# Optimization experiments

Measured on AMD Instinct MI355X. Metric: run time of the kernel, lower is better.

Reference implementation:

```python
import jax, jax.numpy as jnp
import numpy as np
import math

EMBED_DIM = 2048
NUM_HEADS = 16
DEPTH = 12
HEAD_DIM = EMBED_DIM // NUM_HEADS // 2  # 64
LAMBDA_INIT = 0.8 - 0.6 * math.exp(-0.3 * DEPTH)
EPS = 1e-8


def apply_rope(x):
    # x: (b, s, h, d) -- lucidrains interleaved rotary, freqs_for='lang', theta=10000
    b, s, h, d = x.shape
    inv_freq = 1.0 / (10000.0 ** (jnp.arange(0, d, 2, dtype=jnp.float32) / d))
    t = jnp.arange(s, dtype=jnp.float32)
    freqs = t[:, None] * inv_freq[None, :]           # (s, d/2)
    freqs = jnp.repeat(freqs, 2, axis=-1)            # (s, d) pairwise repeat
    cos = jnp.cos(freqs)[None, :, None, :].astype(x.dtype)
    sin = jnp.sin(freqs)[None, :, None, :].astype(x.dtype)
    x1 = x[..., 0::2]
    x2 = x[..., 1::2]
    rot = jnp.stack([-x2, x1], axis=-1).reshape(x.shape)  # rotate_half, interleaved
    return x * cos + rot * sin


def causal_attn(q, k, v):
    # q,k: (b, s, h, d); v: (b, s, h, e). flash_attn_func default scale = d**-0.5
    b, s, h, d = q.shape
    scale = d ** -0.5
    scores = jnp.einsum('bqhd,bkhd->bhqk', q, k) * scale
    mask = jnp.tril(jnp.ones((s, s), dtype=bool))
    scores = jnp.where(mask[None, None], scores, jnp.finfo(scores.dtype).min)
    p = jax.nn.softmax(scores, axis=-1)
    return jnp.einsum('bhqk,bkhe->bqhe', p, v)


def rms_norm(x, w, b):
    var = jnp.mean(jnp.square(x), axis=-1, keepdims=True)
    return x * jax.lax.rsqrt(var + EPS) * w + b


def setup_inputs() -> dict:
    key = jax.random.key(0)
    ks = jax.random.split(key, 11)
    D = EMBED_DIM
    std = D ** -0.5
    return {
        'x': jax.random.normal(ks[0], (2, 2048, D), dtype=jnp.float32),
        'Wq': jax.random.normal(ks[1], (D, D), dtype=jnp.float32) * std,
        'Wk': jax.random.normal(ks[2], (D, D), dtype=jnp.float32) * std,
        'Wv': jax.random.normal(ks[3], (D, D), dtype=jnp.float32) * std,
        'Wo': jax.random.normal(ks[4], (D, D), dtype=jnp.float32) * std,
        'lambda_q1': jax.random.normal(ks[5], (HEAD_DIM,), dtype=jnp.float32) * 0.1,
        'lambda_k1': jax.random.normal(ks[6], (HEAD_DIM,), dtype=jnp.float32) * 0.1,
        'lambda_q2': jax.random.normal(ks[7], (HEAD_DIM,), dtype=jnp.float32) * 0.1,
        'lambda_k2': jax.random.normal(ks[8], (HEAD_DIM,), dtype=jnp.float32) * 0.1,
        'ln_w': jnp.ones((2 * HEAD_DIM,), dtype=jnp.float32),
        'ln_b': jnp.zeros((2 * HEAD_DIM,), dtype=jnp.float32),
    }


def reference(x, Wq, Wk, Wv, Wo, lambda_q1, lambda_k1, lambda_q2, lambda_k2, ln_w, ln_b):
    b, s, D = x.shape
    H, hd = NUM_HEADS, HEAD_DIM
    q = (x @ Wq).reshape(b, s, 2 * H, hd)
    k = (x @ Wk).reshape(b, s, 2 * H, hd)
    v = (x @ Wv).reshape(b, s, H, 2 * hd)
    q = apply_rope(q)
    k = apply_rope(k)
    q = q.reshape(b, s, H, 2, hd)
    k = k.reshape(b, s, H, 2, hd)
    q1, q2 = q[:, :, :, 0], q[:, :, :, 1]
    k1, k2 = k[:, :, :, 0], k[:, :, :, 1]
    attn1 = causal_attn(q1, k1, v)   # (b, s, H, 2*hd)
    attn2 = causal_attn(q2, k2, v)
    lam1 = jnp.exp(jnp.sum(lambda_q1 * lambda_k1))
    lam2 = jnp.exp(jnp.sum(lambda_q2 * lambda_k2))
    lam = lam1 - lam2 + LAMBDA_INIT
    attn = rms_norm(attn1 - lam * attn2, ln_w, ln_b)
    attn = attn * (1.0 - LAMBDA_INIT)
    attn = attn.reshape(b, s, D)
    return attn @ Wo
```

## Files before the change

kernel.cpp:

```cpp
#include <hip/hip_runtime.h>

typedef unsigned short u16;
typedef unsigned int   u32;
typedef short bf16x8 __attribute__((ext_vector_type(8)));
typedef float f32x4  __attribute__((ext_vector_type(4)));

#define SQ 2048
#define DMODEL 2048
#define NROWS 4096
#define LAMBDA_INIT 0.7836057665316245f
#define OUT_SCALE   0.21639423346837552f
#define CSC 0.18033688011112042f

__device__ __forceinline__ float bf2f(u16 u) {
    union { u32 u; float f; } x; x.u = ((u32)u) << 16; return x.f;
}
__device__ __forceinline__ u16 f2bf(float f) {
    union { float f; u32 u; } x; x.f = f;
    u32 r = x.u + 0x7fffu + ((x.u >> 16) & 1u);
    return (u16)(r >> 16);
}

__device__ __forceinline__ void gload_lds16(const void* g, void* l) {
    __builtin_amdgcn_global_load_lds((const __attribute__((address_space(1))) void*)g,
                                     (__attribute__((address_space(3))) void*)l,
                                     16, 0, 0);
}

__global__ __launch_bounds__(256) void transpose_w(const float* __restrict__ W0,
                                                   const float* __restrict__ W1,
                                                   const float* __restrict__ W2,
                                                   const float* __restrict__ W3,
                                                   u16* __restrict__ out) {
    __shared__ float tile[32][33];
    const int z = blockIdx.z;
    const float* W = (z == 0) ? W0 : (z == 1) ? W1 : (z == 2) ? W2 : W3;
    u16* O = out + (size_t)z * DMODEL * DMODEL;
    const int tx = threadIdx.x, ty = threadIdx.y;
    const int bx = blockIdx.x, by = blockIdx.y;
#pragma unroll
    for (int j = 0; j < 4; ++j)
        tile[ty + j * 8][tx] = W[(size_t)(by * 32 + ty + j * 8) * DMODEL + bx * 32 + tx];
    __syncthreads();
#pragma unroll
    for (int j = 0; j < 4; ++j)
        O[(size_t)(bx * 32 + ty + j * 8) * DMODEL + by * 32 + tx] = f2bf(tile[tx][ty + j * 8]);
}

__global__ __launch_bounds__(256) void cvt_x(const float* __restrict__ x, u16* __restrict__ xb) {
    const size_t i = ((size_t)blockIdx.x * 256 + threadIdx.x) * 8;
    float4 a = *(const float4*)(x + i);
    float4 b = *(const float4*)(x + i + 4);
    uint4 o;
    o.x = (u32)f2bf(a.x) | ((u32)f2bf(a.y) << 16);
    o.y = (u32)f2bf(a.z) | ((u32)f2bf(a.w) << 16);
    o.z = (u32)f2bf(b.x) | ((u32)f2bf(b.y) << 16);
    o.w = (u32)f2bf(b.z) | ((u32)f2bf(b.w) << 16);
    *(uint4*)(xb + i) = o;
}

template <bool OUT_BF16>
__global__ __launch_bounds__(256) void gemm_bt(const u16* __restrict__ A,
                                               const u16* __restrict__ Bt0,
                                               void* __restrict__ C0) {
    __shared__ u16 As[128 * 32];
    __shared__ u16 Bs[128 * 32];
    const int tid  = threadIdx.x;
    const int lane = tid & 63, wave = tid >> 6;
    const int wm = wave & 1, wn = wave >> 1;
    const int l15 = lane & 15, quad = lane >> 4;
    const int tm = blockIdx.y * 128, tn = blockIdx.x * 128;
    const u16* Bt = Bt0 + (size_t)blockIdx.z * DMODEL * DMODEL;

    const int r_l = lane >> 2, c_l = lane & 3;

    f32x4 acc[4][4] = {};

    for (int k0 = 0; k0 < DMODEL; k0 += 32) {
#pragma unroll
        for (int c = 0; c < 2; ++c) {
            const int chunk = wave * 2 + c;
            const int row = chunk * 16 + r_l;
            gload_lds16(A  + (size_t)(tm + row) * DMODEL + k0 + c_l * 8, &As[chunk * 512]);
            gload_lds16(Bt + (size_t)(tn + row) * DMODEL + k0 + c_l * 8, &Bs[chunk * 512]);
        }
        __syncthreads();
        bf16x8 af[4], bfr[4];
#pragma unroll
        for (int mb = 0; mb < 4; ++mb)
            af[mb] = *(const bf16x8*)(As + (wm * 64 + mb * 16 + l15) * 32 + quad * 8);
#pragma unroll
        for (int nb = 0; nb < 4; ++nb)
            bfr[nb] = *(const bf16x8*)(Bs + (wn * 64 + nb * 16 + l15) * 32 + quad * 8);
#pragma unroll
        for (int mb = 0; mb < 4; ++mb)
#pragma unroll
            for (int nb = 0; nb < 4; ++nb)
                acc[mb][nb] = __builtin_amdgcn_mfma_f32_16x16x32_bf16(af[mb], bfr[nb], acc[mb][nb], 0, 0, 0);
        __syncthreads();
    }
#pragma unroll
    for (int mb = 0; mb < 4; ++mb)
#pragma unroll
        for (int nb = 0; nb < 4; ++nb)
#pragma unroll
            for (int r = 0; r < 4; ++r) {
                const int row = tm + wm * 64 + mb * 16 + quad * 4 + r;
                const int col = tn + wn * 64 + nb * 16 + l15;
                const float v = acc[mb][nb][r];
                if (OUT_BF16) {
                    u16* C = (u16*)C0 + (size_t)blockIdx.z * NROWS * DMODEL;
                    C[(size_t)row * DMODEL + col] = f2bf(v);
                } else {
                    float* C = (float*)C0;
                    C[(size_t)row * DMODEL + col] = v;
                }
            }
}

__global__ __launch_bounds__(256) void rope_kernel(u16* __restrict__ qw, u16* __restrict__ kw) {
    const int row = blockIdx.x;
    const int spos = row & (SQ - 1);
    u16* buf = blockIdx.y ? kw : qw;
    for (int idx = threadIdx.x; idx < 1024; idx += 256) {
        const int h2 = idx >> 5, i = idx & 31;
        const size_t base = (size_t)row * DMODEL + h2 * 64 + 2 * i;
        const float x1 = bf2f(buf[base]), x2 = bf2f(buf[base + 1]);
        const float f = (float)spos * exp2f(-0.41524101186092034f * (float)i);
        const float c = cosf(f), sn = sinf(f);
        buf[base]     = f2bf(x1 * c - x2 * sn);
        buf[base + 1] = f2bf(x2 * c + x1 * sn);
    }
}

__global__ void lam_kernel(const float* __restrict__ lq1, const float* __restrict__ lk1,
                           const float* __restrict__ lq2, const float* __restrict__ lk2,
                           float* __restrict__ out) {
    const int l = threadIdx.x;
    float v1 = lq1[l] * lk1[l];
    float v2 = lq2[l] * lk2[l];
#pragma unroll
    for (int off = 32; off; off >>= 1) {
        v1 += __shfl_xor(v1, off);
        v2 += __shfl_xor(v2, off);
    }
    if (l == 0) out[0] = __expf(v1) - __expf(v2) + LAMBDA_INIT;
}

__global__ __launch_bounds__(256) void vtrans(const u16* __restrict__ vb, u16* __restrict__ vtg) {
    __shared__ u16 tile[64][72];
    const int bh = blockIdx.z;
    const int b = bh >> 4, h = bh & 15;
    const int s0 = blockIdx.x * 64, d0 = blockIdx.y * 64;
    const size_t rowbase = (size_t)b * SQ;
    const int tid = threadIdx.x;
#pragma unroll
    for (int it = 0; it < 2; ++it) {
        const int slot = it * 256 + tid;
        const int key = slot >> 3, dg = slot & 7;
        *(uint4*)&tile[key][dg * 8] =
            *(const uint4*)(vb + (rowbase + s0 + key) * DMODEL + h * 128 + d0 + dg * 8);
    }
    __syncthreads();
#pragma unroll
    for (int it = 0; it < 2; ++it) {
        const int slot = it * 256 + tid;
        const int d = slot >> 3, kg = slot & 7;
        u16 e[8];
#pragma unroll
        for (int j = 0; j < 8; ++j) e[j] = tile[kg * 8 + j][d];
        uint4 o;
        o.x = (u32)e[0] | ((u32)e[1] << 16);
        o.y = (u32)e[2] | ((u32)e[3] << 16);
        o.z = (u32)e[4] | ((u32)e[5] << 16);
        o.w = (u32)e[6] | ((u32)e[7] << 16);
        *(uint4*)(vtg + ((size_t)bh * 128 + d0 + d) * SQ + s0 + kg * 8) = o;
    }
}

__global__ __launch_bounds__(256) void attn_kernel(const u16* __restrict__ qw,
                                                   const u16* __restrict__ kw,
                                                   const u16* __restrict__ vtg,
                                                   const float* __restrict__ lamp,
                                                   const float* __restrict__ lnw,
                                                   const float* __restrict__ lnb,
                                                   u16* __restrict__ yb) {
    __shared__ u16 Ks[2][64 * 128];
    __shared__ u16 Vts[2][128 * 64];
    __shared__ u16 Pls[4][16 * 72];

    const int tid = threadIdx.x, lane = tid & 63, wave = tid >> 6;
    const int l15 = lane & 15, quad = lane >> 4;
    const int bh = blockIdx.x, b = bh >> 4, h = bh & 15;
    const int pair = blockIdx.y;
    const size_t rowbase = (size_t)b * SQ;
    const int coff = h * 128;
    const float lam = lamp[0];
    const int nt0 = pair + 1;

    int kOff[4], vOff[4];
#pragma unroll
    for (int i = 0; i < 4; ++i) {
        const int cK  = wave * 4 + i;
        const int key = cK * 4 + (lane >> 4);
        const int cg  = (lane & 15) ^ (key & 7);
        kOff[i] = key * DMODEL + coff + cg * 8;
        const int dd  = cK * 8 + (lane >> 3);
        const int kg  = (lane & 7) ^ (lane >> 3);
        vOff[i] = dd * SQ + kg * 8;
    }
    const size_t kBase = rowbase * DMODEL;
    const size_t vBase = (size_t)bh * 128 * SQ;

    auto stageKV = [&](int t0, int d) {
#pragma unroll
        for (int i = 0; i < 4; ++i) {
            gload_lds16(kw + kBase + (size_t)t0 * DMODEL + kOff[i], &Ks[d][(wave * 4 + i) * 512]);
            gload_lds16(vtg + vBase + t0 + vOff[i], &Vts[d][(wave * 4 + i) * 512]);
        }
    };

    int g = 0;
    stageKV(0, 0);

#pragma unroll 1
    for (int s = 0; s < 2; ++s) {
        const int strip = s ? (31 - pair) : pair;
        const int q0 = strip * 64;
        const int nt = strip + 1;

        bf16x8 qf[2][2];
        {
            const size_t qbase = (rowbase + q0 + wave * 16 + l15) * DMODEL + coff + quad * 8;
#pragma unroll
            for (int hf = 0; hf < 2; ++hf)
#pragma unroll
                for (int ks = 0; ks < 2; ++ks)
                    qf[hf][ks] = *(const bf16x8*)(qw + qbase + hf * 64 + ks * 32);
        }

        f32x4 O[2][8] = {};
        float mm[2][4], ll[2][4];
#pragma unroll
        for (int hf = 0; hf < 2; ++hf)
#pragma unroll
            for (int r = 0; r < 4; ++r) { mm[hf][r] = -1e30f; ll[hf][r] = 0.f; }

        for (int t = 0; t < nt; ++t, ++g) {
            const int t0 = t * 64;
            __syncthreads();
            {
                const int gn = g + 1;
                if (gn < 33) {
                    const int tn = (gn < nt0) ? gn : gn - nt0;
                    stageKV(tn * 64, gn & 1);
                }
            }
            const u16* __restrict__ KsB = Ks[g & 1];
            const u16* __restrict__ VtB = Vts[g & 1];
            const bool maskt = (t == nt - 1);

#pragma unroll
            for (int hf = 0; hf < 2; ++hf) {
                f32x4 S[4] = {};
#pragma unroll
                for (int nb = 0; nb < 4; ++nb)
#pragma unroll
                    for (int ks = 0; ks < 2; ++ks) {
                        const int cgp = (hf * 8 + ks * 4 + quad) ^ (l15 & 7);
                        bf16x8 kf = *(const bf16x8*)&KsB[(nb * 16 + l15) * 128 + cgp * 8];
                        S[nb] = __builtin_amdgcn_mfma_f32_16x16x32_bf16(qf[hf][ks], kf, S[nb], 0, 0, 0);
                    }
                float mt[4];
#pragma unroll
                for (int r = 0; r < 4; ++r) mt[r] = -1e30f;
#pragma unroll
                for (int nb = 0; nb < 4; ++nb)
#pragma unroll
                    for (int r = 0; r < 4; ++r) {
                        float sv = S[nb][r] * CSC;
                        if (maskt && (nb * 16 + l15 > wave * 16 + quad * 4 + r)) sv = -1e30f;
                        S[nb][r] = sv;
                        mt[r] = fmaxf(mt[r], sv);
                    }
#pragma unroll
                for (int r = 0; r < 4; ++r)
#pragma unroll
                    for (int off = 1; off < 16; off <<= 1)
                        mt[r] = fmaxf(mt[r], __shfl_xor(mt[r], off));
                float alpha[4], ps[4];
#pragma unroll
                for (int r = 0; r < 4; ++r) {
                    const float mn = fmaxf(mm[hf][r], mt[r]);
                    alpha[r] = exp2f(mm[hf][r] - mn);
                    mm[hf][r] = mn;
                    ps[r] = 0.f;
                }
#pragma unroll
                for (int nb = 0; nb < 4; ++nb)
#pragma unroll
                    for (int r = 0; r < 4; ++r) {
                        const float p = exp2f(S[nb][r] - mm[hf][r]);
                        const u32 pu = __builtin_bit_cast(u32, p);
                        ps[r] += __builtin_bit_cast(float, pu & 0xffff0000u);
                        Pls[wave][(quad * 4 + r) * 72 + nb * 16 + l15] = (u16)(pu >> 16);
                    }
#pragma unroll
                for (int r = 0; r < 4; ++r) {
#pragma unroll
                    for (int off = 1; off < 16; off <<= 1) ps[r] += __shfl_xor(ps[r], off);
                    ll[hf][r] = ll[hf][r] * alpha[r] + ps[r];
                }
#pragma unroll
                for (int nb = 0; nb < 8; ++nb)
#pragma unroll
                    for (int r = 0; r < 4; ++r) O[hf][nb][r] *= alpha[r];
                bf16x8 pf[2];
#pragma unroll
                for (int ks = 0; ks < 2; ++ks)
                    pf[ks] = *(const bf16x8*)&Pls[wave][l15 * 72 + ks * 32 + quad * 8];
#pragma unroll
                for (int nb = 0; nb < 8; ++nb)
#pragma unroll
                    for (int ks = 0; ks < 2; ++ks) {
                        const int kgp = (ks * 4 + quad) ^ (l15 & 7);
                        bf16x8 vf = *(const bf16x8*)&VtB[(nb * 16 + l15) * 64 + kgp * 8];
                        O[hf][nb] = __builtin_amdgcn_mfma_f32_16x16x32_bf16(pf[ks], vf, O[hf][nb], 0, 0, 0);
                    }
            }
        }

        float inl1[4], inl2[4];
#pragma unroll
        for (int r = 0; r < 4; ++r) { inl1[r] = 1.f / ll[0][r]; inl2[r] = 1.f / ll[1][r]; }
        float vv[8][4], ss[4] = {0.f, 0.f, 0.f, 0.f};
#pragma unroll
        for (int nb = 0; nb < 8; ++nb)
#pragma unroll
            for (int r = 0; r < 4; ++r) {
                const float v = O[0][nb][r] * inl1[r] - lam * O[1][nb][r] * inl2[r];
                vv[nb][r] = v;
                ss[r] += v * v;
            }
#pragma unroll
        for (int r = 0; r < 4; ++r) {
#pragma unroll
            for (int off = 1; off < 16; off <<= 1) ss[r] += __shfl_xor(ss[r], off);
            ss[r] = rsqrtf(ss[r] * (1.f / 128.f) + 1e-8f) * OUT_SCALE;
        }
#pragma unroll
        for (int nb = 0; nb < 8; ++nb) {
            const int d = nb * 16 + l15;
            const float w = lnw[d], bb = lnb[d] * OUT_SCALE;
#pragma unroll
            for (int r = 0; r < 4; ++r) {
                const size_t row = rowbase + q0 + wave * 16 + quad * 4 + r;
                yb[row * DMODEL + coff + d] = f2bf(vv[nb][r] * ss[r] * w + bb);
            }
        }
    }
}

#define WT_OFF   0ull
#define XB_OFF   33554432ull
#define Q_OFF    50331648ull
#define K_OFF    67108864ull
#define V_OFF    83886080ull
#define VT_OFF   100663296ull
#define LAM_OFF  117440512ull
#define WS_NEED  117440768ull

extern "C" void kernel_launch(void* const* d_in, const int* in_sizes, int n_in,
                              void* d_out, int out_size, void* d_ws, size_t ws_size,
                              hipStream_t stream) {
    if (ws_size < WS_NEED) return;
    const float* x   = (const float*)d_in[0];
    const float* Wq  = (const float*)d_in[1];
    const float* Wk  = (const float*)d_in[2];
    const float* Wv  = (const float*)d_in[3];
    const float* Wo  = (const float*)d_in[4];
    const float* lq1 = (const float*)d_in[5];
    const float* lk1 = (const float*)d_in[6];
    const float* lq2 = (const float*)d_in[7];
    const float* lk2 = (const float*)d_in[8];
    const float* lnw = (const float*)d_in[9];
    const float* lnb = (const float*)d_in[10];

    char* ws = (char*)d_ws;
    u16* wt  = (u16*)(ws + WT_OFF);
    u16* xb  = (u16*)(ws + XB_OFF);
    u16* qb  = (u16*)(ws + Q_OFF);
    u16* kb  = (u16*)(ws + K_OFF);
    u16* vb  = (u16*)(ws + V_OFF);
    u16* vtg = (u16*)(ws + VT_OFF);
    float* lam = (float*)(ws + LAM_OFF);
    float* out = (float*)d_out;

    transpose_w<<<dim3(64, 64, 4), dim3(32, 8, 1), 0, stream>>>(Wq, Wk, Wv, Wo, wt);
    cvt_x<<<dim3(4096), dim3(256), 0, stream>>>(x, xb);
    gemm_bt<true><<<dim3(16, 32, 3), dim3(256), 0, stream>>>(xb, wt, qb);
    rope_kernel<<<dim3(4096, 2), dim3(256), 0, stream>>>(qb, kb);
    lam_kernel<<<dim3(1), dim3(64), 0, stream>>>(lq1, lk1, lq2, lk2, lam);
    vtrans<<<dim3(32, 2, 32), dim3(256), 0, stream>>>(vb, vtg);
    attn_kernel<<<dim3(32, 16), dim3(256), 0, stream>>>(qb, kb, vtg, lam, lnw, lnb, xb);
    gemm_bt<false><<<dim3(16, 32, 1), dim3(256), 0, stream>>>(xb, wt + 3ull * DMODEL * DMODEL, out);
}
```

Baseline: 560.5 us.

## Replace double-buffered K/V staging with single buffer and extra barrier

Removes the ping-pong K/V LDS buffers and the cross-strip prefetch of the next tile. Each tile is now loaded at the start of its iteration, followed by a barrier, with a second barrier after compute. This halves K/V shared memory, which may allow more resident blocks per CU. The cost is that load latency is no longer overlapped with MFMA work and each tile adds a barrier.

```diff
diff --git a/kernel.cpp b/kernel.cpp
--- a/kernel.cpp
+++ b/kernel.cpp
@@ -185,8 +185,8 @@
                                                    const float* __restrict__ lnw,
                                                    const float* __restrict__ lnb,
                                                    u16* __restrict__ yb) {
-    __shared__ u16 Ks[2][64 * 128];
-    __shared__ u16 Vts[2][128 * 64];
+    __shared__ u16 Ks[64 * 128];
+    __shared__ u16 Vts[128 * 64];
     __shared__ u16 Pls[4][16 * 72];
 
     const int tid = threadIdx.x, lane = tid & 63, wave = tid >> 6;
@@ -196,7 +196,6 @@
     const size_t rowbase = (size_t)b * SQ;
     const int coff = h * 128;
     const float lam = lamp[0];
-    const int nt0 = pair + 1;
 
     int kOff[4], vOff[4];
 #pragma unroll
@@ -212,16 +211,13 @@
     const size_t kBase = rowbase * DMODEL;
     const size_t vBase = (size_t)bh * 128 * SQ;
 
-    auto stageKV = [&](int t0, int d) {
+    auto stageKV = [&](int t0) {
 #pragma unroll
         for (int i = 0; i < 4; ++i) {
-            gload_lds16(kw + kBase + (size_t)t0 * DMODEL + kOff[i], &Ks[d][(wave * 4 + i) * 512]);
-            gload_lds16(vtg + vBase + t0 + vOff[i], &Vts[d][(wave * 4 + i) * 512]);
+            gload_lds16(kw + kBase + (size_t)t0 * DMODEL + kOff[i], &Ks[(wave * 4 + i) * 512]);
+            gload_lds16(vtg + vBase + t0 + vOff[i], &Vts[(wave * 4 + i) * 512]);
         }
     };
-
-    int g = 0;
-    stageKV(0, 0);
 
 #pragma unroll 1
     for (int s = 0; s < 2; ++s) {
@@ -246,18 +242,10 @@
 #pragma unroll
             for (int r = 0; r < 4; ++r) { mm[hf][r] = -1e30f; ll[hf][r] = 0.f; }
 
-        for (int t = 0; t < nt; ++t, ++g) {
+        for (int t = 0; t < nt; ++t) {
             const int t0 = t * 64;
+            stageKV(t0);
             __syncthreads();
-            {
-                const int gn = g + 1;
-                if (gn < 33) {
-                    const int tn = (gn < nt0) ? gn : gn - nt0;
-                    stageKV(tn * 64, gn & 1);
-                }
-            }
-            const u16* __restrict__ KsB = Ks[g & 1];
-            const u16* __restrict__ VtB = Vts[g & 1];
             const bool maskt = (t == nt - 1);
 
 #pragma unroll
@@ -268,7 +256,7 @@
 #pragma unroll
                     for (int ks = 0; ks < 2; ++ks) {
                         const int cgp = (hf * 8 + ks * 4 + quad) ^ (l15 & 7);
-                        bf16x8 kf = *(const bf16x8*)&KsB[(nb * 16 + l15) * 128 + cgp * 8];
+                        bf16x8 kf = *(const bf16x8*)&Ks[(nb * 16 + l15) * 128 + cgp * 8];
                         S[nb] = __builtin_amdgcn_mfma_f32_16x16x32_bf16(qf[hf][ks], kf, S[nb], 0, 0, 0);
                     }
                 float mt[4];
@@ -324,10 +312,11 @@
 #pragma unroll
                     for (int ks = 0; ks < 2; ++ks) {
                         const int kgp = (ks * 4 + quad) ^ (l15 & 7);
-                        bf16x8 vf = *(const bf16x8*)&VtB[(nb * 16 + l15) * 64 + kgp * 8];
+                        bf16x8 vf = *(const bf16x8*)&Vts[(nb * 16 + l15) * 64 + kgp * 8];
                         O[hf][nb] = __builtin_amdgcn_mfma_f32_16x16x32_bf16(pf[ks], vf, O[hf][nb], 0, 0, 0);
                     }
             }
+            __syncthreads();
         }
 
         float inl1[4], inl2[4];
```

New measurement: 498.6 us. 11.1% less time.
